# Kernel tuning notes

Measured on AMD Instinct MI355X. Metric: run time of the kernel, lower is better.

Reference implementation:

```python
import jax, jax.numpy as jnp
import numpy as np

F4_MAX = 6.0      # float4 e2m1 max magnitude
F8_MAX = 448.0    # float8 e4m3 max magnitude
BLOCK = 16        # nvfp4 block size along reduction dim


def _fp4_e2m1_rne(v):
    """Round v to the nearest float4 e2m1 value, ties-to-even.
    Representable magnitudes: {0, 0.5, 1, 1.5, 2, 3, 4, 6}."""
    s = jnp.sign(v)
    a = jnp.clip(jnp.abs(v), 0.0, F4_MAX)
    # exponent of the quantization step: subnormals and [1,2) share step 0.5
    e = jnp.clip(jnp.floor(jnp.log2(jnp.maximum(a, 1.0))), 0.0, 2.0)
    step = jnp.exp2(e - 1.0)  # 0.5, 1.0 or 2.0
    q = jnp.round(a / step) * step  # jnp.round is round-half-to-even
    return s * jnp.clip(q, 0.0, F4_MAX)


def _nvfp4_quant_dequant(x, global_scale):
    """scaled_fp4_quant followed by dequant (== what the scaled fp4 GEMM
    with alpha = 1/(gs_a*gs_w) computes per operand)."""
    lead, K = x.shape[:-1], x.shape[-1]
    xb = x.reshape(*lead, K // BLOCK, BLOCK)
    amax = jnp.max(jnp.abs(xb), axis=-1, keepdims=True)            # per-block amax
    scale = (amax * (global_scale / F4_MAX))
    scale = scale.astype(jnp.float8_e4m3fn).astype(jnp.float32)    # e4m3 block scale
    safe = jnp.where(scale > 0.0, scale, 1.0)
    q = _fp4_e2m1_rne(xb * (global_scale / safe))                  # fp4 codes (as floats)
    dq = q * safe / global_scale                                   # dequantized values
    return dq.reshape(x.shape)


def setup_inputs() -> dict:
    key = jax.random.key(0)
    k1, k2, k3 = jax.random.split(key, 3)
    B, S, K, N = 4, 2048, 4096, 4096
    x = jax.random.normal(k1, (B, S, K), dtype=jnp.float32)
    W = jax.random.normal(k2, (N, K), dtype=jnp.float32) * 0.02
    bias = jax.random.normal(k3, (N,), dtype=jnp.float32) * 0.02
    return {"x": x, "W": W, "bias": bias}


def reference(x, W, bias):
    # per-tensor global scales (FLOAT8_E4M3_MAX * FLOAT4_E2M1_MAX / amax)
    x_gs = (F8_MAX * F4_MAX) / jnp.max(jnp.abs(x)).astype(jnp.float32)
    w_gs = (F8_MAX * F4_MAX) / jnp.max(jnp.abs(W)).astype(jnp.float32)
    x_dq = _nvfp4_quant_dequant(x, x_gs)   # [B,S,K]
    w_dq = _nvfp4_quant_dequant(W, w_gs)   # [N,K]
    out = jnp.einsum('bsk,nk->bsn', x_dq, w_dq) + bias
    return out.astype(x.dtype)
```

## Files before the change

kernel.cpp:

```cpp
#include <hip/hip_runtime.h>
#include <stdint.h>

typedef unsigned short u16;
typedef __bf16 bf16x8 __attribute__((ext_vector_type(8)));
typedef float floatx16 __attribute__((ext_vector_type(16)));

#define TM 128
#define TN 128
#define BK 64

__global__ void amax_both_k(const float4* __restrict__ x, long nx4,
                            const float4* __restrict__ w, long nw4,
                            unsigned* slots, int gx) {
    const float4* src; long n4; int bid, nb; unsigned* slot;
    if ((int)blockIdx.x < gx) { src = x; n4 = nx4; bid = blockIdx.x; nb = gx; slot = slots; }
    else { src = w; n4 = nw4; bid = blockIdx.x - gx; nb = gridDim.x - gx; slot = slots + 1; }
    float m = 0.0f;
    long stride = (long)nb * blockDim.x;
    for (long i = (long)bid * blockDim.x + threadIdx.x; i < n4; i += stride) {
        float4 v = src[i];
        m = fmaxf(m, fmaxf(fmaxf(fabsf(v.x), fabsf(v.y)), fmaxf(fabsf(v.z), fabsf(v.w))));
    }
    #pragma unroll
    for (int off = 32; off > 0; off >>= 1)
        m = fmaxf(m, __shfl_down(m, off, 64));
    __shared__ float sm[4];
    int lane = threadIdx.x & 63, wv = threadIdx.x >> 6;
    if (lane == 0) sm[wv] = m;
    __syncthreads();
    if (threadIdx.x == 0) {
        m = fmaxf(fmaxf(sm[0], sm[1]), fmaxf(sm[2], sm[3]));
        atomicMax(slot, __float_as_uint(m));
    }
}

__device__ __forceinline__ float e4m3_rne(float v) {
    unsigned u = __float_as_uint(v);
    u += 0x7FFFFu + ((u >> 20) & 1u);
    float hi = __uint_as_float(u & 0xFFF00000u);
    float lo = rintf(v * 512.0f) * 0.001953125f;
    return (v < 0.015625f) ? lo : hi;
}

__device__ __forceinline__ float fp4_rne(float x) {
    float a = fminf(fabsf(x), 6.0f);
    unsigned u = __float_as_uint(a);
    u += 0x1FFFFFu + ((u >> 22) & 1u);
    float hi = __uint_as_float(u & 0xFFC00000u);
    float lo = rintf(a + a) * 0.5f;
    float q = (a < 1.0f) ? lo : hi;
    return copysignf(q, x);
}

__device__ __forceinline__ unsigned pack2(float d0, float d1) {
    return (__float_as_uint(d0) >> 16) | (__float_as_uint(d1) & 0xFFFF0000u);
}

__global__ void quant_both_k(const float* __restrict__ x, const float* __restrict__ W,
                             u16* __restrict__ Aq, u16* __restrict__ Bq,
                             const unsigned* __restrict__ slots, long nbx, long nbtot) {
    long b = (long)blockIdx.x * blockDim.x + threadIdx.x;
    if (b >= nbtot) return;
    const float* src; u16* dst; float ag;
    if (b < nbx) { src = x + b * 16; dst = Aq + b * 16; ag = __uint_as_float(slots[0]); }
    else { long c = b - nbx; src = W + c * 16; dst = Bq + c * 16; ag = __uint_as_float(slots[1]); }
    float gs = 2688.0f / ag;
    float t  = gs / 6.0f;
    const float4* p = (const float4*)src;
    float4 v0 = p[0], v1 = p[1], v2 = p[2], v3 = p[3];
    float am = 0.0f;
    am = fmaxf(am, fmaxf(fmaxf(fabsf(v0.x), fabsf(v0.y)), fmaxf(fabsf(v0.z), fabsf(v0.w))));
    am = fmaxf(am, fmaxf(fmaxf(fabsf(v1.x), fabsf(v1.y)), fmaxf(fabsf(v1.z), fabsf(v1.w))));
    am = fmaxf(am, fmaxf(fmaxf(fabsf(v2.x), fabsf(v2.y)), fmaxf(fabsf(v2.z), fabsf(v2.w))));
    am = fmaxf(am, fmaxf(fmaxf(fabsf(v3.x), fabsf(v3.y)), fmaxf(fabsf(v3.z), fabsf(v3.w))));
    float sf = e4m3_rne(am * t);
    float r = gs / (sf > 0.0f ? sf : 1.0f);
    uint4 o0, o1;
    o0.x = pack2(fp4_rne(v0.x * r) * sf, fp4_rne(v0.y * r) * sf);
    o0.y = pack2(fp4_rne(v0.z * r) * sf, fp4_rne(v0.w * r) * sf);
    o0.z = pack2(fp4_rne(v1.x * r) * sf, fp4_rne(v1.y * r) * sf);
    o0.w = pack2(fp4_rne(v1.z * r) * sf, fp4_rne(v1.w * r) * sf);
    o1.x = pack2(fp4_rne(v2.x * r) * sf, fp4_rne(v2.y * r) * sf);
    o1.y = pack2(fp4_rne(v2.z * r) * sf, fp4_rne(v2.w * r) * sf);
    o1.z = pack2(fp4_rne(v3.x * r) * sf, fp4_rne(v3.y * r) * sf);
    o1.w = pack2(fp4_rne(v3.z * r) * sf, fp4_rne(v3.w * r) * sf);
    uint4* q = (uint4*)dst;
    q[0] = o0; q[1] = o1;
}

__global__ __launch_bounds__(256) void gemm_k(
    const u16* __restrict__ A, const u16* __restrict__ B,
    const float* __restrict__ bias, const unsigned* __restrict__ scal,
    float* __restrict__ out, int M, int N, int K)
{
    __shared__ u16 As[TM * BK];
    __shared__ u16 Bs[TN * BK];
    const int tid  = threadIdx.x;
    const int lane = tid & 63;
    const int wv   = tid >> 6;
    const int tileM = blockIdx.y * TM;
    const int tileN = blockIdx.x * TN;
    const int wm = (wv >> 1) * 64;
    const int wn = (wv & 1) * 64;
    const int r32  = lane & 31;
    const int half = lane >> 5;

    floatx16 acc[2][2] = {};

    const int srow_base = wv * 32;
    const int sr = lane >> 3;
    const int sc = lane & 7;

    for (int k0 = 0; k0 < K; k0 += BK) {
        #pragma unroll
        for (int i = 0; i < 4; i++) {
            int r = srow_base + i * 8 + sr;
            int g = sc ^ (r & 7);
            const u16* ga = A + (size_t)(tileM + r) * K + k0 + g * 8;
            const u16* gb = B + (size_t)(tileN + r) * K + k0 + g * 8;
            __builtin_amdgcn_global_load_lds(
                (const __attribute__((address_space(1))) void*)ga,
                (__attribute__((address_space(3))) void*)(As + (srow_base + i * 8) * BK),
                16, 0, 0);
            __builtin_amdgcn_global_load_lds(
                (const __attribute__((address_space(1))) void*)gb,
                (__attribute__((address_space(3))) void*)(Bs + (srow_base + i * 8) * BK),
                16, 0, 0);
        }
        __syncthreads();
        #pragma unroll
        for (int t = 0; t < 4; t++) {
            int ch = t * 2 + half;
            bf16x8 af[2], bfr[2];
            #pragma unroll
            for (int i = 0; i < 2; i++) {
                int m = wm + i * 32 + r32;
                af[i] = *(const bf16x8*)(As + m * BK + ((ch ^ (m & 7)) * 8));
                int n = wn + i * 32 + r32;
                bfr[i] = *(const bf16x8*)(Bs + n * BK + ((ch ^ (n & 7)) * 8));
            }
            #pragma unroll
            for (int i = 0; i < 2; i++)
                #pragma unroll
                for (int j = 0; j < 2; j++)
                    acc[i][j] = __builtin_amdgcn_mfma_f32_32x32x16_bf16(
                        af[i], bfr[j], acc[i][j], 0, 0, 0);
        }
        __syncthreads();
    }

    float ax = __uint_as_float(scal[0]);
    float aw = __uint_as_float(scal[1]);
    float gsx = 2688.0f / ax, gsw = 2688.0f / aw;
    float alpha = 1.0f / (gsx * gsw);

    #pragma unroll
    for (int j = 0; j < 2; j++) {
        int n = tileN + wn + j * 32 + r32;
        float bv = bias[n];
        #pragma unroll
        for (int i = 0; i < 2; i++) {
            int mbase = tileM + wm + i * 32 + half * 4;
            #pragma unroll
            for (int reg = 0; reg < 16; reg++) {
                int row = (reg & 3) + 8 * (reg >> 2);
                out[(size_t)(mbase + row) * N + n] = acc[i][j][reg] * alpha + bv;
            }
        }
    }
}

extern "C" void kernel_launch(void* const* d_in, const int* in_sizes, int n_in,
                              void* d_out, int out_size, void* d_ws, size_t ws_size,
                              hipStream_t stream) {
    const float* x    = (const float*)d_in[0];
    const float* W    = (const float*)d_in[1];
    const float* bias = (const float*)d_in[2];
    float* out = (float*)d_out;

    const int N = in_sizes[2];
    const int K = in_sizes[1] / N;
    const int M = in_sizes[0] / K;

    unsigned* scal = (unsigned*)d_ws;
    u16* Aq = (u16*)((char*)d_ws + 256);
    u16* Bq = Aq + (size_t)M * K;

    hipMemsetAsync(scal, 0, 8, stream);

    const int GX = 2048, GW = 1024;
    hipLaunchKernelGGL(amax_both_k, dim3(GX + GW), dim3(256), 0, stream,
                       (const float4*)x, (long)M * K / 4,
                       (const float4*)W, (long)N * K / 4, scal, GX);

    long nbx = (long)M * K / 16;
    long nbw = (long)N * K / 16;
    hipLaunchKernelGGL(quant_both_k, dim3((unsigned)((nbx + nbw + 255) / 256)), dim3(256), 0, stream,
                       x, W, Aq, Bq, scal, nbx, nbx + nbw);

    hipLaunchKernelGGL(gemm_k, dim3(N / TN, M / TM), dim3(256), 0, stream,
                       Aq, Bq, bias, scal, out, M, N, K);
}
```

Measured before the change: 588.6 us.

## Rewrite GEMM as 256x256 double-buffered pipelined kernel with XCD-aware tile swizzle

```diff
diff --git a/kernel.cpp b/kernel.cpp
--- a/kernel.cpp
+++ b/kernel.cpp
@@ -3,11 +3,7 @@
 
 typedef unsigned short u16;
 typedef __bf16 bf16x8 __attribute__((ext_vector_type(8)));
-typedef float floatx16 __attribute__((ext_vector_type(16)));
-
-#define TM 128
-#define TN 128
-#define BK 64
+typedef float floatx4 __attribute__((ext_vector_type(4)));
 
 __global__ void amax_both_k(const float4* __restrict__ x, long nx4,
                             const float4* __restrict__ w, long nw4,
@@ -88,65 +84,134 @@
     q[0] = o0; q[1] = o1;
 }
 
-__global__ __launch_bounds__(256) void gemm_k(
+#define KTILE 64
+
+#define SFENCE() __builtin_amdgcn_sched_barrier(0)
+#define BAR() do { asm volatile("" ::: "memory"); SFENCE(); \
+    __builtin_amdgcn_s_barrier(); SFENCE(); asm volatile("" ::: "memory"); } while (0)
+
+#define STAGE_SLOT(GS, LS) do { \
+    __builtin_amdgcn_global_load_lds((const __attribute__((address_space(1))) void*)(GS), \
+        (__attribute__((address_space(3))) void*)(LS), 16, 0, 0); \
+    __builtin_amdgcn_global_load_lds((const __attribute__((address_space(1))) void*)((GS) + row64K), \
+        (__attribute__((address_space(3))) void*)((LS) + 4096), 16, 0, 0); \
+} while (0)
+
+#define LDA(CUR, MH) do { \
+    _Pragma("unroll") for (int mf = 0; mf < 4; ++mf) { \
+        const u16* p_ = aB + (CUR) * 16384 + ((MH) * 64 + mf * 16) * 64; \
+        af[mf][0] = *(const bf16x8*)(p_ + ca0 * 8); \
+        af[mf][1] = *(const bf16x8*)(p_ + ca1 * 8); \
+    } } while (0)
+
+#define LDB(CUR, NH) do { \
+    _Pragma("unroll") for (int nf = 0; nf < 2; ++nf) { \
+        const u16* p_ = bB + (CUR) * 16384 + ((NH) * 32 + nf * 16) * 64; \
+        bf[(NH)*2+nf][0] = *(const bf16x8*)(p_ + ca0 * 8); \
+        bf[(NH)*2+nf][1] = *(const bf16x8*)(p_ + ca1 * 8); \
+    } } while (0)
+
+#define QUAD(MH, NH) do { \
+    _Pragma("unroll") for (int ks = 0; ks < 2; ++ks) \
+    _Pragma("unroll") for (int mf = 0; mf < 4; ++mf) \
+    _Pragma("unroll") for (int nf = 0; nf < 2; ++nf) \
+        acc[(MH)*4+mf][(NH)*2+nf] = __builtin_amdgcn_mfma_f32_16x16x32_bf16( \
+            af[mf][ks], bf[(NH)*2+nf][ks], acc[(MH)*4+mf][(NH)*2+nf], 0, 0, 0); \
+} while (0)
+
+#define TILE(CUR, S) do { \
+    const u16* gA1 = Ag + (size_t)(((S)+1 < NT) ? (S)+1 : NT-1) * KTILE; \
+    const u16* gB2 = Bg + (size_t)(((S)+2 < NT) ? (S)+2 : NT-1) * KTILE; \
+    u16* lA1 = Al + ((CUR)^1) * 16384; \
+    u16* lB2 = Bl + (CUR) * 16384; \
+     \
+    LDA(CUR, 0); LDB(CUR, 0); \
+    STAGE_SLOT(gA1, lA1); \
+    BAR(); \
+    __builtin_amdgcn_s_setprio(1); QUAD(0, 0); __builtin_amdgcn_s_setprio(0); \
+    BAR(); \
+     \
+    LDB(CUR, 1); \
+    STAGE_SLOT(gA1 + halfGA, lA1 + 8192); \
+    BAR(); \
+    __builtin_amdgcn_s_setprio(1); QUAD(0, 1); __builtin_amdgcn_s_setprio(0); \
+    BAR(); \
+     \
+    LDA(CUR, 1); \
+    STAGE_SLOT(gB2, lB2); \
+    BAR(); \
+    __builtin_amdgcn_s_setprio(1); QUAD(1, 0); __builtin_amdgcn_s_setprio(0); \
+    BAR(); \
+     \
+    STAGE_SLOT(gB2 + halfGA, lB2 + 8192); \
+    BAR(); \
+    __builtin_amdgcn_s_setprio(1); QUAD(1, 1); __builtin_amdgcn_s_setprio(0); \
+    SFENCE(); \
+    asm volatile("s_waitcnt vmcnt(4)" ::: "memory"); \
+    BAR(); \
+} while (0)
+
+__global__ __launch_bounds__(512, 2) void gemm_k(
     const u16* __restrict__ A, const u16* __restrict__ B,
     const float* __restrict__ bias, const unsigned* __restrict__ scal,
     float* __restrict__ out, int M, int N, int K)
 {
-    __shared__ u16 As[TM * BK];
-    __shared__ u16 Bs[TN * BK];
-    const int tid  = threadIdx.x;
-    const int lane = tid & 63;
-    const int wv   = tid >> 6;
-    const int tileM = blockIdx.y * TM;
-    const int tileN = blockIdx.x * TN;
-    const int wm = (wv >> 1) * 64;
-    const int wn = (wv & 1) * 64;
-    const int r32  = lane & 31;
-    const int half = lane >> 5;
-
-    floatx16 acc[2][2] = {};
-
-    const int srow_base = wv * 32;
-    const int sr = lane >> 3;
-    const int sc = lane & 7;
-
-    for (int k0 = 0; k0 < K; k0 += BK) {
-        #pragma unroll
-        for (int i = 0; i < 4; i++) {
-            int r = srow_base + i * 8 + sr;
-            int g = sc ^ (r & 7);
-            const u16* ga = A + (size_t)(tileM + r) * K + k0 + g * 8;
-            const u16* gb = B + (size_t)(tileN + r) * K + k0 + g * 8;
-            __builtin_amdgcn_global_load_lds(
-                (const __attribute__((address_space(1))) void*)ga,
-                (__attribute__((address_space(3))) void*)(As + (srow_base + i * 8) * BK),
-                16, 0, 0);
-            __builtin_amdgcn_global_load_lds(
-                (const __attribute__((address_space(1))) void*)gb,
-                (__attribute__((address_space(3))) void*)(Bs + (srow_base + i * 8) * BK),
-                16, 0, 0);
-        }
-        __syncthreads();
-        #pragma unroll
-        for (int t = 0; t < 4; t++) {
-            int ch = t * 2 + half;
-            bf16x8 af[2], bfr[2];
-            #pragma unroll
-            for (int i = 0; i < 2; i++) {
-                int m = wm + i * 32 + r32;
-                af[i] = *(const bf16x8*)(As + m * BK + ((ch ^ (m & 7)) * 8));
-                int n = wn + i * 32 + r32;
-                bfr[i] = *(const bf16x8*)(Bs + n * BK + ((ch ^ (n & 7)) * 8));
-            }
-            #pragma unroll
-            for (int i = 0; i < 2; i++)
-                #pragma unroll
-                for (int j = 0; j < 2; j++)
-                    acc[i][j] = __builtin_amdgcn_mfma_f32_32x32x16_bf16(
-                        af[i], bfr[j], acc[i][j], 0, 0, 0);
-        }
-        __syncthreads();
+    __shared__ u16 As[2 * 256 * 64];
+    __shared__ u16 Bs[2 * 256 * 64];
+
+    const int tid = threadIdx.x;
+    const int l   = tid & 63;
+    const int wv  = tid >> 6;
+    const int wm  = wv >> 2;
+    const int wn  = wv & 3;
+
+    const int nTM = M / 256, nTN = N / 256;
+    const int nwg = nTM * nTN;
+    const int orig = blockIdx.x;
+    const int xcd = orig & 7, lid = orig >> 3;
+    const int q8 = nwg >> 3, r8 = nwg & 7;
+    const int swz = (xcd < r8 ? xcd * (q8 + 1) : r8 * (q8 + 1) + (xcd - r8) * q8) + lid;
+    const long tileM = (long)(swz % nTM) * 256;
+    const long tileN = (long)(swz / nTM) * 256;
+
+    const int srow  = tid >> 3;
+    const int sslot = tid & 7;
+    const int schunk = sslot ^ (srow & 7);
+    const size_t row64K = (size_t)64 * K;
+    const size_t halfGA = (size_t)128 * K;
+    const u16* Ag = A + (size_t)(tileM + srow) * K + schunk * 8;
+    const u16* Bg = B + (size_t)(tileN + srow) * K + schunk * 8;
+    u16* Al = As + wv * 512;
+    u16* Bl = Bs + wv * 512;
+
+    const int lr = l & 15;
+    const int hi = l >> 4;
+    const int ca0 = hi ^ (lr & 7);
+    const int ca1 = ca0 ^ 4;
+    const u16* aB = As + (wm * 128 + lr) * 64;
+    const u16* bB = Bs + (wn * 64 + lr) * 64;
+
+    floatx4 acc[8][4] = {};
+    bf16x8 af[4][2], bf[4][2];
+
+    const int NT = K / KTILE;
+
+    STAGE_SLOT(Bg, Bl);
+    STAGE_SLOT(Bg + halfGA, Bl + 8192);
+    STAGE_SLOT(Ag, Al);
+    STAGE_SLOT(Ag + halfGA, Al + 8192);
+    {
+        const u16* gB1 = Bg + ((1 < NT) ? KTILE : 0);
+        STAGE_SLOT(gB1, Bl + 16384);
+        STAGE_SLOT(gB1 + halfGA, Bl + 16384 + 8192);
+    }
+    SFENCE();
+    asm volatile("s_waitcnt vmcnt(4)" ::: "memory");
+    BAR();
+
+    for (int s = 0; s < NT; s += 2) {
+        TILE(0, s);
+        TILE(1, s + 1);
     }
 
     float ax = __uint_as_float(scal[0]);
@@ -155,17 +220,15 @@
     float alpha = 1.0f / (gsx * gsw);
 
     #pragma unroll
-    for (int j = 0; j < 2; j++) {
-        int n = tileN + wn + j * 32 + r32;
-        float bv = bias[n];
+    for (int nq = 0; nq < 4; ++nq) {
+        const long col = tileN + wn * 64 + nq * 16 + lr;
+        const float bv = bias[col];
         #pragma unroll
-        for (int i = 0; i < 2; i++) {
-            int mbase = tileM + wm + i * 32 + half * 4;
+        for (int mq = 0; mq < 8; ++mq) {
+            const long r0 = tileM + wm * 128 + mq * 16 + hi * 4;
             #pragma unroll
-            for (int reg = 0; reg < 16; reg++) {
-                int row = (reg & 3) + 8 * (reg >> 2);
-                out[(size_t)(mbase + row) * N + n] = acc[i][j][reg] * alpha + bv;
-            }
+            for (int reg = 0; reg < 4; ++reg)
+                out[(size_t)(r0 + reg) * N + col] = acc[mq][nq][reg] * alpha + bv;
         }
     }
 }
@@ -198,6 +261,6 @@
     hipLaunchKernelGGL(quant_both_k, dim3((unsigned)((nbx + nbw + 255) / 256)), dim3(256), 0, stream,
                        x, W, Aq, Bq, scal, nbx, nbx + nbw);
 
-    hipLaunchKernelGGL(gemm_k, dim3(N / TN, M / TM), dim3(256), 0, stream,
+    hipLaunchKernelGGL(gemm_k, dim3((M / 256) * (N / 256)), dim3(512), 0, stream,
                        Aq, Bq, bias, scal, out, M, N, K);
 }
```

Measured after the change: 581.2 us. Within noise of the previous version (-1.3%).
